# Kernel optimization log

Measured on AMD Instinct MI355X. Metric: run time of the kernel, lower is better.

## Reference

```python
import jax, jax.numpy as jnp
import numpy as np
from jax import lax

B, N, C = 16, 1024, 768
HID = 128           # route_hidden_dim (Cattn bottleneck + router hidden)
OUT = 2304          # qkv out_feature


def setup_inputs() -> dict:
    key = jax.random.key(0)
    ks = jax.random.split(key, 16)
    s = 0.02
    return {
        "input":  jax.random.normal(ks[0], (B, N, C), jnp.float32),
        "H": 32,
        "W": 32,
        "input2": jax.random.normal(ks[1], (B, N, C), jnp.float32),
        # qkv linear
        "qkv_w": jax.random.normal(ks[2], (OUT, C), jnp.float32) * s,
        "qkv_b": jax.random.normal(ks[3], (OUT,), jnp.float32) * s,
        # Cattn (vida_refine): fc1 -> dwconv -> gelu -> fc2
        "fc1_w": jax.random.normal(ks[4], (HID, C), jnp.float32) * s,
        "fc1_b": jnp.zeros((HID,), jnp.float32),
        "dw_w":  jax.random.normal(ks[5], (HID, 1, 3, 3), jnp.float32) * np.sqrt(2.0 / 9.0),
        "dw_b":  jnp.zeros((HID,), jnp.float32),
        "fc2_w": jax.random.normal(ks[6], (C, HID), jnp.float32) * s,
        "fc2_b": jnp.zeros((C,), jnp.float32),
        # router MLP: 1 -> HID -> 2
        "r1_w": jax.random.normal(ks[7], (HID, 1), jnp.float32) * s,
        "r1_b": jnp.zeros((HID,), jnp.float32),
        "r2_w": jax.random.normal(ks[8], (2, HID), jnp.float32) * s,
        "r2_b": jnp.zeros((2,), jnp.float32),
    }


def _linear(x, w, b):
    return jnp.einsum("bnc,oc->bno", x, w) + b


def _cattn(x, H, W, fc1_w, fc1_b, dw_w, dw_b, fc2_w, fc2_b):
    # fc1 -> depthwise 3x3 conv over HxW -> GELU(exact) -> fc2
    x = _linear(x, fc1_w, fc1_b)                       # [B,N,HID]
    b, n, h = x.shape
    xi = x.transpose(0, 2, 1).reshape(b, h, H, W)      # [B,HID,H,W]
    xi = lax.conv_general_dilated(
        xi, dw_w, window_strides=(1, 1), padding="SAME",
        feature_group_count=h,
        dimension_numbers=("NCHW", "OIHW", "NCHW"),
    ) + dw_b[None, :, None, None]
    x = xi.reshape(b, h, n).transpose(0, 2, 1)         # [B,N,HID]
    x = jax.nn.gelu(x, approximate=False)              # torch nn.GELU default = erf
    return _linear(x, fc2_w, fc2_b)                    # [B,N,C]


def _get_logit(inp, refine_x2):
    # cosine sim between per-batch token-mean of `inp` and refine_x2, then
    # per-batch min-max normalization (skipped when max == min)
    mean = jnp.mean(inp, axis=1, keepdims=True)        # [B,1,C]
    dot = jnp.sum(refine_x2 * mean, axis=-1, keepdims=True)
    n1 = jnp.linalg.norm(mean, axis=-1, keepdims=True)
    n2 = jnp.linalg.norm(refine_x2, axis=-1, keepdims=True)
    csim = dot / (n1 * n2)                             # [B,N,1]
    mn = jnp.min(csim, axis=1, keepdims=True)
    mx = jnp.max(csim, axis=1, keepdims=True)
    rng = mx - mn
    return jnp.where(rng != 0, (csim - mn) / jnp.where(rng != 0, rng, 1.0), csim)


def reference(input, H, W, input2, qkv_w, qkv_b, fc1_w, fc1_b, dw_w, dw_b,
              fc2_w, fc2_b, r1_w, r1_b, r2_w, r2_b):
    q1 = _linear(input, qkv_w, qkv_b)                              # [B,N,OUT]
    refine_x2 = input2 + _cattn(input2, H, W, fc1_w, fc1_b, dw_w, dw_b, fc2_w, fc2_b)
    q2 = _linear(refine_x2, qkv_w, qkv_b)                          # [B,N,OUT]
    csim = _get_logit(input, refine_x2)                            # [B,N,1]
    h = jax.nn.relu(_linear(csim, r1_w, r1_b))                     # [B,N,HID]
    logits = jax.nn.sigmoid(_linear(h, r2_w, r2_b))                # [B,N,2]
    # gumbel_softmax(hard=False, tau=1) with a fixed key for determinism
    g = jax.random.gumbel(jax.random.key(42), logits.shape, logits.dtype)
    router = jax.nn.softmax(logits + g, axis=-1)[:, :, 0]          # [B,N]
    return (q1, q2, router)
```

## Files before the change

kernel.cpp:

```cpp
#include <hip/hip_runtime.h>
#include <cstdint>
#include <cstddef>

#define BQ 16
#define NT 1024
#define CH 768
#define HIDN 128
#define OUTF 2304
#define MTOT (BQ*NT)

typedef __attribute__((ext_vector_type(4))) float f32x4;
typedef __attribute__((ext_vector_type(8))) short short8;

__device__ __forceinline__ unsigned short f2bf(float f){
  unsigned u = __float_as_uint(f);
  u += 0x7FFFu + ((u >> 16) & 1u);
  return (unsigned short)(u >> 16);
}
__device__ __forceinline__ float bf2f(unsigned short h){
  return __uint_as_float(((unsigned)h) << 16);
}

__device__ __forceinline__ void gload16(const void* g, void* l){
  __builtin_amdgcn_global_load_lds((const __attribute__((address_space(1))) void*)g,
                                   (__attribute__((address_space(3))) void*)l, 16, 0, 0);
}

__device__ __forceinline__ void mfma16(f32x4& d, short8 a, short8 b){
  asm volatile("v_mfma_f32_16x16x32_bf16 %0, %1, %2, %0" : "+v"(d) : "v"(a), "v"(b));
}

__global__ void k_f2bf_all(const float* __restrict__ in0, const float* __restrict__ in1,
                           const float* __restrict__ in2, const float* __restrict__ in3,
                           const float* __restrict__ in4,
                           unsigned short* __restrict__ o0, unsigned short* __restrict__ o1,
                           unsigned short* __restrict__ o2, unsigned short* __restrict__ o3,
                           unsigned short* __restrict__ o4)
{
  const long step = (long)2048 * 256 * 4;
  for (long i = (long)(blockIdx.x * 256 + threadIdx.x) * 4; i < 27131904L; i += step){
    const float* s; unsigned short* d; long off;
    if      (i < 12582912L){ s = in0; d = o0; off = i; }
    else if (i < 25165824L){ s = in1; d = o1; off = i - 12582912L; }
    else if (i < 26935296L){ s = in2; d = o2; off = i - 25165824L; }
    else if (i < 27033600L){ s = in3; d = o3; off = i - 26935296L; }
    else                   { s = in4; d = o4; off = i - 27033600L; }
    float4 v = *reinterpret_cast<const float4*>(s + off);
    ushort4 o;
    o.x = f2bf(v.x); o.y = f2bf(v.y); o.z = f2bf(v.z); o.w = f2bf(v.w);
    *reinterpret_cast<ushort4*>(d + off) = o;
  }
}

#define STAGE(matB_, buf_, h_, t_) { \
    const unsigned short* g_ = ((matB_) ? Bbase : Abase) + (size_t)(h_)*128*K + (size_t)(t_)*64; \
    char* d_ = ldsWaveDst + (matB_)*65536 + (buf_)*32768 + (h_)*16384; \
    gload16(g_, d_); \
    gload16(g_ + rowK64, d_ + 8192); \
  }

#define PH_OPEN() \
    asm volatile("s_barrier" ::: "memory"); \
    asm volatile("s_waitcnt lgkmcnt(0)" ::: "memory"); \
    __builtin_amdgcn_sched_barrier(0); \
    __builtin_amdgcn_s_setprio(1);

#define PH_CLOSE() \
    __builtin_amdgcn_s_setprio(0); \
    asm volatile("s_barrier" ::: "memory");

#define MF16(mb, nb, BV) \
    _Pragma("unroll") \
    for (int ks = 0; ks < 2; ++ks) \
      _Pragma("unroll") \
      for (int mf = 0; mf < 4; ++mf) \
        _Pragma("unroll") \
        for (int nf = 0; nf < 2; ++nf) \
          mfma16(acc[(mb)+mf][(nb)+nf], av[mf][ks], BV[nf][ks]);

#define TILE(t_, b_) { \
    const int t = (t_); const int b = (b_); \
    _Pragma("unroll") for (int mf = 0; mf < 4; ++mf){ av[mf][0]=ldA(b,mf,0); av[mf][1]=ldA(b,mf,1); } \
    _Pragma("unroll") for (int nf = 0; nf < 2; ++nf){ b0v[nf][0]=ldB(b,nf,0); b0v[nf][1]=ldB(b,nf,1); } \
    if (t+1 < T) STAGE(0, b^1, 1, t+1); \
    PH_OPEN(); MF16(0,0,b0v); PH_CLOSE(); \
    _Pragma("unroll") for (int nf = 0; nf < 2; ++nf){ b1v[nf][0]=ldB(b,2+nf,0); b1v[nf][1]=ldB(b,2+nf,1); } \
    if (t+1 < T) STAGE(1, b^1, 0, t+1); \
    PH_OPEN(); MF16(0,2,b1v); PH_CLOSE(); \
    _Pragma("unroll") for (int mf = 0; mf < 4; ++mf){ av[mf][0]=ldA(b,4+mf,0); av[mf][1]=ldA(b,4+mf,1); } \
    if (t+2 < T) STAGE(0, b, 0, t+2); \
    PH_OPEN(); MF16(4,2,b1v); PH_CLOSE(); \
    if (t+2 < T) STAGE(1, b, 1, t+2); \
    PH_OPEN(); MF16(4,0,b0v); \
    __builtin_amdgcn_s_setprio(0); \
    if (t+2 < T) { asm volatile("s_waitcnt vmcnt(4)" ::: "memory"); } \
    else         { asm volatile("s_waitcnt vmcnt(0)" ::: "memory"); } \
    asm volatile("s_barrier" ::: "memory"); \
  }

template<int T>
__device__ __forceinline__
void gemm256_body(char* lds8,
                  const unsigned short* __restrict__ A,
                  const unsigned short* __restrict__ B,
                  const float* __restrict__ bias,
                  float* __restrict__ C,
                  int N, int K, int nbn, int bid, int nwg)
{
  const int tid = threadIdx.x;
  const int ln = tid & 63, wv = tid >> 6;
  const int wm = wv >> 2, wn = wv & 3;
  const int llo = ln & 15, lhi = ln >> 4;

  const int cpx = nwg >> 3;
  const int swz = (bid & 7) * cpx + (bid >> 3);
  const int bm = swz / nbn, bn = swz % nbn;
  const int m0 = bm * 256, n0 = bn * 256;

  const int srow = tid >> 3;
  const int sslot = (tid & 7) ^ (srow & 7);
  const unsigned short* Abase = A + (size_t)(m0 + srow) * K + sslot * 8;
  const unsigned short* Bbase = B + (size_t)(n0 + srow) * K + sslot * 8;
  const size_t rowK64 = (size_t)64 * K;
  char* ldsWaveDst = lds8 + (wv << 10);

  const int swz0 = ((lhi ^ (ln & 7)) << 4);
  const char* aRd0 = lds8 + (wm*64 + llo)*128 + swz0;
  const char* aRd1 = lds8 + (wm*64 + llo)*128 + (swz0 ^ 64);
  const char* bRd0 = lds8 + 65536 + (wn*32 + llo)*128 + swz0;
  const char* bRd1 = lds8 + 65536 + (wn*32 + llo)*128 + (swz0 ^ 64);

  auto ldA = [&](int b, int mf, int ks) -> short8 {
    const char* p = (ks ? aRd1 : aRd0) + b*32768 + (mf>>2)*16384 + (mf&3)*2048;
    return *reinterpret_cast<const short8*>(p);
  };
  auto ldB = [&](int b, int nf, int ks) -> short8 {
    const char* p = (ks ? bRd1 : bRd0) + b*32768 + (nf>>1)*16384 + (nf&1)*2048;
    return *reinterpret_cast<const short8*>(p);
  };

  f32x4 acc[8][4];
  #pragma unroll
  for (int m = 0; m < 8; ++m)
    #pragma unroll
    for (int n = 0; n < 4; ++n) acc[m][n] = 0.0f;

  STAGE(0, 0, 0, 0);
  STAGE(1, 0, 1, 0);
  STAGE(0, 0, 1, 0);
  STAGE(1, 0, 0, 0);
  STAGE(0, 1, 0, 1);
  STAGE(1, 1, 1, 1);
  asm volatile("s_waitcnt vmcnt(4)" ::: "memory");
  asm volatile("s_barrier" ::: "memory");

  short8 av[4][2], b0v[2][2], b1v[2][2];
  #pragma unroll 1
  for (int t0 = 0; t0 < T; t0 += 2){
    TILE(t0,   0);
    TILE(t0+1, 1);
  }

  asm volatile("s_nop 7\n\ts_nop 7\n\ts_nop 7" ::: );

  #pragma unroll
  for (int mf = 0; mf < 8; ++mf){
    const int row = m0 + (mf>>2)*128 + wm*64 + (mf&3)*16 + lhi*4;
    #pragma unroll
    for (int j = 0; j < 4; ++j){
      #pragma unroll
      for (int nf = 0; nf < 4; ++nf){
        const int col = n0 + (nf>>1)*128 + wn*32 + (nf&1)*16 + llo;
        C[(size_t)(row + j) * N + col] = acc[mf][nf][j] + bias[col];
      }
    }
  }
}

__device__ __forceinline__
void fc1_body(char* lds, const unsigned short* __restrict__ A,
              const unsigned short* __restrict__ B,
              const float* __restrict__ bias, unsigned short* __restrict__ Cb, int fb)
{
  const int tid = threadIdx.x;
  if (tid >= 256){
    #pragma unroll 1
    for (int i = 0; i < 24; ++i){ __syncthreads(); __syncthreads(); }
    return;
  }
  unsigned short (*sA)[32] = (unsigned short(*)[32])lds;
  unsigned short (*sB)[32] = (unsigned short(*)[32])(lds + 8192);
  const int wv = tid >> 6, ln = tid & 63;
  const int wr = wv >> 1, wc = wv & 1;
  const int lhi = ln >> 4, llo = ln & 15;
  const int m0 = fb * 128;
  const int N = 128, K = 768;

  f32x4 acc[4][4];
  #pragma unroll
  for (int m = 0; m < 4; ++m)
    #pragma unroll
    for (int n = 0; n < 4; ++n) acc[m][n] = 0.0f;

  const int lrow = ln >> 2;
  const int lk8  = (ln & 3) * 8;

  #pragma unroll 1
  for (int kt = 0; kt < 768; kt += 32){
    #pragma unroll
    for (int cc = 0; cc < 2; ++cc){
      int c = wv * 2 + cc;
      gload16(A + (size_t)(m0 + c*16 + lrow) * K + kt + lk8, &sA[c*16][0]);
      gload16(B + (size_t)(c*16 + lrow) * K + kt + lk8, &sB[c*16][0]);
    }
    __syncthreads();

    short8 av[4], bv[4];
    #pragma unroll
    for (int m = 0; m < 4; ++m)
      av[m] = *reinterpret_cast<const short8*>(&sA[wr*64 + m*16 + llo][lhi*8]);
    #pragma unroll
    for (int n = 0; n < 4; ++n)
      bv[n] = *reinterpret_cast<const short8*>(&sB[wc*64 + n*16 + llo][lhi*8]);

    #pragma unroll
    for (int m = 0; m < 4; ++m)
      #pragma unroll
      for (int n = 0; n < 4; ++n)
        mfma16(acc[m][n], bv[n], av[m]);
    __syncthreads();
  }

  asm volatile("s_nop 7\n\ts_nop 7\n\ts_nop 7" ::: );

  float4 bias4[4];
  #pragma unroll
  for (int n = 0; n < 4; ++n)
    bias4[n] = *reinterpret_cast<const float4*>(&bias[wc*64 + n*16 + lhi*4]);

  #pragma unroll
  for (int m = 0; m < 4; ++m){
    const int row = m0 + wr*64 + m*16 + llo;
    #pragma unroll
    for (int n = 0; n < 4; ++n){
      const int colbase = wc*64 + n*16 + lhi*4;
      ushort4 o;
      o.x = f2bf(acc[m][n][0] + bias4[n].x);
      o.y = f2bf(acc[m][n][1] + bias4[n].y);
      o.z = f2bf(acc[m][n][2] + bias4[n].z);
      o.w = f2bf(acc[m][n][3] + bias4[n].w);
      *reinterpret_cast<ushort4*>(&Cb[(size_t)row * N + colbase]) = o;
    }
  }
}

__device__ __forceinline__
void mean_body(char* lds, const unsigned short* __restrict__ x1b,
               float* __restrict__ meanb, float* __restrict__ n1p, int mbid)
{
  float (*tmp)[128] = (float(*)[128])lds;
  const int b = mbid / 6, cg = mbid % 6;
  const int tid = threadIdx.x;
  const int oct = tid & 15, rg = tid >> 4;
  const unsigned short* ip = x1b + (size_t)b*NT*CH + (size_t)rg*32*CH + cg*128 + oct*8;

  float s[8];
  #pragma unroll
  for (int j = 0; j < 8; ++j) s[j] = 0.f;
  #pragma unroll 4
  for (int r = 0; r < 32; ++r){
    short8 v = *reinterpret_cast<const short8*>(ip + (size_t)r*CH);
    #pragma unroll
    for (int j = 0; j < 8; ++j) s[j] += bf2f((unsigned short)v[j]);
  }
  #pragma unroll
  for (int j = 0; j < 8; ++j) tmp[rg][oct*8 + j] = s[j];
  __syncthreads();

  if (tid < 128){
    float m = 0.f;
    #pragma unroll
    for (int g = 0; g < 32; ++g) m += tmp[g][tid];
    m *= (1.0f/1024.0f);
    meanb[b*CH + cg*128 + tid] = m;
    float q = m * m;
    for (int off = 32; off; off >>= 1) q += __shfl_down(q, off, 64);
    if ((tid & 63) == 0) n1p[b*12 + cg*2 + (tid >> 6)] = q;
  }
}

__device__ __forceinline__ void threefry(unsigned k0, unsigned k1, unsigned x0, unsigned x1,
                                         unsigned& o0, unsigned& o1){
  unsigned ks2 = k0 ^ k1 ^ 0x1BD11BDAu;
  x0 += k0; x1 += k1;
#define TFR(r) { x0 += x1; x1 = (x1 << r) | (x1 >> (32 - r)); x1 ^= x0; }
  TFR(13) TFR(15) TFR(26) TFR(6)  x0 += k1;  x1 += ks2 + 1u;
  TFR(17) TFR(29) TFR(16) TFR(24) x0 += ks2; x1 += k0 + 2u;
  TFR(13) TFR(15) TFR(26) TFR(6)  x0 += k0;  x1 += k1 + 3u;
  TFR(17) TFR(29) TFR(16) TFR(24) x0 += k1;  x1 += ks2 + 4u;
  TFR(13) TFR(15) TFR(26) TFR(6)  x0 += ks2; x1 += k0 + 5u;
#undef TFR
  o0 = x0; o1 = x1;
}

__device__ __forceinline__ float gumbel_from_bits(unsigned bits){
  float f = __uint_as_float((bits >> 9) | 0x3F800000u) - 1.0f;
  const float TINY = 1.17549435e-38f;
  float u = fmaxf(TINY, f + TINY);
  return -logf(-logf(u));
}

__device__ __forceinline__
void router_body(char* lds, const float* __restrict__ part, const float* __restrict__ n1p,
                 const float* __restrict__ r1w, const float* __restrict__ r1b,
                 const float* __restrict__ r2w, const float* __restrict__ r2b,
                 float* __restrict__ out, int b)
{
  float* cs   = (float*)lds;
  float* red  = (float*)(lds + 4096);
  float* w1s  = (float*)(lds + 4096 + 64);
  float* b1s  = w1s + HIDN;
  float* w20s = b1s + HIDN;
  float* w21s = w20s + HIDN;
  const int tid = threadIdx.x;
  if (tid < HIDN){
    w1s[tid]  = r1w[tid];
    b1s[tid]  = r1b[tid];
    w20s[tid] = r2w[tid];
    w21s[tid] = r2w[HIDN + tid];
  }
  float n1s = 0.f;
  #pragma unroll
  for (int s = 0; s < 12; ++s) n1s += n1p[b*12 + s];
  float n1 = sqrtf(n1s);
  float lmin = 3.4e38f, lmax = -3.4e38f;
  #pragma unroll
  for (int j = 0; j < 2; ++j){
    int tk = tid + j*512;
    int t = b*NT + tk;
    float dot = 0.f, q = 0.f;
    #pragma unroll
    for (int s = 0; s < 12; ++s){
      dot += part[(size_t)s * MTOT + t];
      q   += part[(size_t)(12 + s) * MTOT + t];
    }
    float v = dot / (n1 * sqrtf(q));
    cs[tk] = v;
    lmin = fminf(lmin, v); lmax = fmaxf(lmax, v);
  }
  int ln = tid & 63, wv = tid >> 6;
  for (int off = 32; off; off >>= 1){
    lmin = fminf(lmin, __shfl_down(lmin, off, 64));
    lmax = fmaxf(lmax, __shfl_down(lmax, off, 64));
  }
  if (ln == 0){ red[wv] = lmin; red[8+wv] = lmax; }
  __syncthreads();
  float mn = red[0], mx = red[8];
  #pragma unroll
  for (int s = 1; s < 8; ++s){ mn = fminf(mn, red[s]); mx = fmaxf(mx, red[8+s]); }
  float rng = mx - mn;
  bool nz = (rng != 0.0f);

  const float r2b0 = r2b[0], r2b1 = r2b[1];
  float v[2], l0[2], l1[2];
  #pragma unroll
  for (int j = 0; j < 2; ++j){
    float c0 = cs[tid + j*512];
    v[j] = nz ? (c0 - mn) / rng : c0;
    l0[j] = r2b0; l1[j] = r2b1;
  }
  for (int k = 0; k < HIDN; ++k){
    float a = w1s[k], bb = b1s[k], c0 = w20s[k], c1 = w21s[k];
    #pragma unroll
    for (int j = 0; j < 2; ++j){
      float hh = fmaxf(v[j] * a + bb, 0.f);
      l0[j] += hh * c0;
      l1[j] += hh * c1;
    }
  }
  #pragma unroll
  for (int j = 0; j < 2; ++j){
    float s0 = 1.f / (1.f + expf(-l0[j]));
    float s1 = 1.f / (1.f + expf(-l1[j]));
    int t = b*NT + tid + j*512;
    unsigned o0, o1;
    threefry(0u, 42u, 0u, (unsigned)(2*t),     o0, o1);
    float g0 = gumbel_from_bits(o0 ^ o1);
    threefry(0u, 42u, 0u, (unsigned)(2*t + 1), o0, o1);
    float g1 = gumbel_from_bits(o0 ^ o1);
    out[t] = 1.f / (1.f + expf((s1 + g1) - (s0 + g0)));
  }
}

__global__ __launch_bounds__(512, 2)
void k_combo1(const unsigned short* __restrict__ xrb, const unsigned short* __restrict__ w1b,
              const float* __restrict__ fc1_b, unsigned short* __restrict__ t1dst,
              const unsigned short* __restrict__ x1b,
              float* __restrict__ meanb, float* __restrict__ n1p)
{
  __shared__ __align__(1024) char lds8[131072];
  const int bid = blockIdx.x;
  if (bid < 128){
    fc1_body(lds8, xrb, w1b, fc1_b, t1dst, bid);
  } else {
    mean_body(lds8, x1b, meanb, n1p, bid - 128);
  }
}

__global__ __launch_bounds__(512, 2)
void k_combo2(const unsigned short* __restrict__ Aall, const unsigned short* __restrict__ wqb,
              const float* __restrict__ qkv_b, float* __restrict__ q1q2,
              const float* __restrict__ part, const float* __restrict__ n1p,
              const float* __restrict__ r1w, const float* __restrict__ r1b,
              const float* __restrict__ r2w, const float* __restrict__ r2b,
              float* __restrict__ router)
{
  __shared__ __align__(1024) char lds8[131072];
  const int bid = blockIdx.x;
  if (bid < 1152){
    gemm256_body<CH/64>(lds8, Aall, wqb, qkv_b, q1q2, OUTF, CH, OUTF/256, bid, 1152);
  } else {
    router_body(lds8, part, n1p, r1w, r1b, r2w, r2b, router, bid - 1152);
  }
}

__global__ __launch_bounds__(256, 2)
void k_gemm_fc2(const unsigned short* __restrict__ A, const unsigned short* __restrict__ B,
                const float* __restrict__ bias, const unsigned short* __restrict__ addb,
                unsigned short* __restrict__ Cb,
                const float* __restrict__ meanb, float* __restrict__ part,
                int M, int N, int K)
{
  __shared__ unsigned short sA[128][32];
  __shared__ unsigned short sB[128][32];
  const int tid = threadIdx.x;
  const int wv = tid >> 6, ln = tid & 63;
  const int wr = wv >> 1, wc = wv & 1;
  const int lhi = ln >> 4, llo = ln & 15;
  const int m0 = blockIdx.x * 128, n0 = blockIdx.y * 128;

  f32x4 acc[4][4];
  #pragma unroll
  for (int m = 0; m < 4; ++m)
    #pragma unroll
    for (int n = 0; n < 4; ++n) acc[m][n] = 0.0f;

  const int lrow = ln >> 2;
  const int lk8  = (ln & 3) * 8;

  for (int kt = 0; kt < K; kt += 32){
    #pragma unroll
    for (int cc = 0; cc < 2; ++cc){
      int c = wv * 2 + cc;
      gload16(A + (size_t)(m0 + c*16 + lrow) * K + kt + lk8, &sA[c*16][0]);
      gload16(B + (size_t)(n0 + c*16 + lrow) * K + kt + lk8, &sB[c*16][0]);
    }
    __syncthreads();

    short8 av[4], bv[4];
    #pragma unroll
    for (int m = 0; m < 4; ++m)
      av[m] = *reinterpret_cast<const short8*>(&sA[wr*64 + m*16 + llo][lhi*8]);
    #pragma unroll
    for (int n = 0; n < 4; ++n)
      bv[n] = *reinterpret_cast<const short8*>(&sB[wc*64 + n*16 + llo][lhi*8]);

    #pragma unroll
    for (int m = 0; m < 4; ++m)
      #pragma unroll
      for (int n = 0; n < 4; ++n)
        mfma16(acc[m][n], bv[n], av[m]);
    __syncthreads();
  }

  asm volatile("s_nop 7\n\ts_nop 7\n\ts_nop 7" ::: );

  float4 bias4[4];
  #pragma unroll
  for (int n = 0; n < 4; ++n)
    bias4[n] = *reinterpret_cast<const float4*>(&bias[n0 + wc*64 + n*16 + lhi*4]);

  const int bb = m0 >> 10;
  const float* mp = meanb + bb * CH;
  float4 mp4[4];
  #pragma unroll
  for (int n = 0; n < 4; ++n)
    mp4[n] = *reinterpret_cast<const float4*>(&mp[n0 + wc*64 + n*16 + lhi*4]);

  #pragma unroll
  for (int m = 0; m < 4; ++m){
    const int row = m0 + wr*64 + m*16 + llo;
    float dsum = 0.f, qsum = 0.f;
    #pragma unroll
    for (int n = 0; n < 4; ++n){
      const int colbase = n0 + wc*64 + n*16 + lhi*4;
      ushort4 a4 = *reinterpret_cast<const ushort4*>(&addb[(size_t)row * N + colbase]);
      float v0 = acc[m][n][0] + bias4[n].x + bf2f(a4.x);
      float v1 = acc[m][n][1] + bias4[n].y + bf2f(a4.y);
      float v2 = acc[m][n][2] + bias4[n].z + bf2f(a4.z);
      float v3 = acc[m][n][3] + bias4[n].w + bf2f(a4.w);
      ushort4 o; o.x = f2bf(v0); o.y = f2bf(v1); o.z = f2bf(v2); o.w = f2bf(v3);
      *reinterpret_cast<ushort4*>(&Cb[(size_t)row * N + colbase]) = o;
      dsum += v0*mp4[n].x + v1*mp4[n].y + v2*mp4[n].z + v3*mp4[n].w;
      qsum += v0*v0 + v1*v1 + v2*v2 + v3*v3;
    }
    dsum += __shfl_xor(dsum, 16, 64);  qsum += __shfl_xor(qsum, 16, 64);
    dsum += __shfl_xor(dsum, 32, 64);  qsum += __shfl_xor(qsum, 32, 64);
    if (ln < 16){
      const int slot = blockIdx.y * 2 + wc;
      part[(size_t)slot * MTOT + row] = dsum;
      part[(size_t)(12 + slot) * MTOT + row] = qsum;
    }
  }
}

__global__ void k_dwgelu(const unsigned short* __restrict__ t1b, const float* __restrict__ dww,
                         const float* __restrict__ dwb, unsigned short* __restrict__ t2)
{
  int idx = blockIdx.x * blockDim.x + threadIdx.x;
  int hq = idx & 31; int t = idx >> 5;
  int h = hq * 4;
  int n = t & (NT-1); int b = t >> 10;
  int y = n >> 5, x = n & 31;

  float w[4][9];
  #pragma unroll
  for (int i = 0; i < 4; ++i)
    #pragma unroll
    for (int k = 0; k < 9; ++k) w[i][k] = dww[(h+i)*9 + k];

  float a0 = dwb[h+0], a1 = dwb[h+1], a2 = dwb[h+2], a3 = dwb[h+3];
  #pragma unroll
  for (int dy = -1; dy <= 1; ++dy){
    int yy = y + dy; if ((unsigned)yy >= 32u) continue;
    #pragma unroll
    for (int dx = -1; dx <= 1; ++dx){
      int xx = x + dx; if ((unsigned)xx >= 32u) continue;
      ushort4 v = *reinterpret_cast<const ushort4*>(&t1b[((size_t)b*NT + yy*32 + xx)*HIDN + h]);
      int k = (dy+1)*3 + (dx+1);
      a0 += bf2f(v.x) * w[0][k]; a1 += bf2f(v.y) * w[1][k];
      a2 += bf2f(v.z) * w[2][k]; a3 += bf2f(v.w) * w[3][k];
    }
  }
  const float is2 = 0.70710678118654752440f;
  a0 = 0.5f*a0*(1.0f + erff(a0*is2));
  a1 = 0.5f*a1*(1.0f + erff(a1*is2));
  a2 = 0.5f*a2*(1.0f + erff(a2*is2));
  a3 = 0.5f*a3*(1.0f + erff(a3*is2));
  ushort4 o; o.x = f2bf(a0); o.y = f2bf(a1); o.z = f2bf(a2); o.w = f2bf(a3);
  *reinterpret_cast<ushort4*>(&t2[(size_t)t*HIDN + h]) = o;
}

extern "C" void kernel_launch(void* const* d_in, const int* in_sizes, int n_in,
                              void* d_out, int out_size, void* d_ws, size_t ws_size,
                              hipStream_t stream)
{
  (void)in_sizes; (void)n_in; (void)out_size;
  const float* input  = (const float*)d_in[0];
  const float* input2 = (const float*)d_in[3];
  const float* qkv_w  = (const float*)d_in[4];
  const float* qkv_b  = (const float*)d_in[5];
  const float* fc1_w  = (const float*)d_in[6];
  const float* fc1_b  = (const float*)d_in[7];
  const float* dw_w   = (const float*)d_in[8];
  const float* dw_b   = (const float*)d_in[9];
  const float* fc2_w  = (const float*)d_in[10];
  const float* fc2_b  = (const float*)d_in[11];
  const float* r1_w   = (const float*)d_in[12];
  const float* r1_b   = (const float*)d_in[13];
  const float* r2_w   = (const float*)d_in[14];
  const float* r2_b   = (const float*)d_in[15];

  float* q1 = (float*)d_out;
  float* router = q1 + (size_t)2 * MTOT * OUTF;

  if (ws_size < 67000000u) return;

  char* ws = (char*)d_ws;
  unsigned short* x1b = (unsigned short*)ws; ws += (size_t)MTOT*CH*2;
  unsigned short* xrb = (unsigned short*)ws; ws += (size_t)MTOT*CH*2;
  unsigned short* wqb = (unsigned short*)ws; ws += (size_t)OUTF*CH*2;
  unsigned short* w1b = (unsigned short*)ws; ws += (size_t)HIDN*CH*2;
  unsigned short* w2b = (unsigned short*)ws; ws += (size_t)CH*HIDN*2;
  unsigned short* t1b = (unsigned short*)ws; ws += (size_t)MTOT*HIDN*4;
  unsigned short* t2  = (unsigned short*)ws; ws += (size_t)MTOT*HIDN*2;
  float*          mb  = (float*)ws;          ws += (size_t)BQ*CH*4;
  float*          n1p = (float*)ws;          ws += 1024;
  float*          part= (float*)t1b;

  k_f2bf_all<<<dim3(2048), 256, 0, stream>>>(
      input, input2, qkv_w, fc1_w, fc2_w, x1b, xrb, wqb, w1b, w2b);

  unsigned short* t1dst = t1b + (size_t)MTOT*HIDN;
  k_combo1<<<dim3(224), 512, 0, stream>>>(
      xrb, w1b, fc1_b, t1dst, x1b, mb, n1p);

  k_dwgelu<<<dim3(MTOT*32/256), 256, 0, stream>>>(t1dst, dw_w, dw_b, t2);

  k_gemm_fc2<<<dim3(MTOT/128, CH/128), 256, 0, stream>>>(
      t2, w2b, fc2_b, xrb, xrb, mb, part, MTOT, CH, HIDN);

  k_combo2<<<dim3(1168), 512, 0, stream>>>(
      x1b, wqb, qkv_b, q1, part, n1p, r1_w, r1_b, r2_w, r2_b, router);
}
```

Measured before the change: 227.2 us.

## Fuse bf16 conversion, fc1 and mean into one kernel reading fp32 directly

Merges the fp32-to-bf16 conversion kernel with the fc1 GEMM and token-mean kernel into a single launch. fc1 and the mean now read the fp32 inputs directly, converting in registers before staging to LDS. The conversion of fc1_w is dropped and the remaining conversion blocks run alongside them. This removes one launch and the serial dependency between the conversion and fc1/mean, at the cost of fc1 reading twice as many bytes and losing the async global-to-LDS loads.

```diff
diff --git a/kernel.cpp b/kernel.cpp
--- a/kernel.cpp
+++ b/kernel.cpp
@@ -30,26 +30,11 @@
   asm volatile("v_mfma_f32_16x16x32_bf16 %0, %1, %2, %0" : "+v"(d) : "v"(a), "v"(b));
 }
 
-__global__ void k_f2bf_all(const float* __restrict__ in0, const float* __restrict__ in1,
-                           const float* __restrict__ in2, const float* __restrict__ in3,
-                           const float* __restrict__ in4,
-                           unsigned short* __restrict__ o0, unsigned short* __restrict__ o1,
-                           unsigned short* __restrict__ o2, unsigned short* __restrict__ o3,
-                           unsigned short* __restrict__ o4)
-{
-  const long step = (long)2048 * 256 * 4;
-  for (long i = (long)(blockIdx.x * 256 + threadIdx.x) * 4; i < 27131904L; i += step){
-    const float* s; unsigned short* d; long off;
-    if      (i < 12582912L){ s = in0; d = o0; off = i; }
-    else if (i < 25165824L){ s = in1; d = o1; off = i - 12582912L; }
-    else if (i < 26935296L){ s = in2; d = o2; off = i - 25165824L; }
-    else if (i < 27033600L){ s = in3; d = o3; off = i - 26935296L; }
-    else                   { s = in4; d = o4; off = i - 27033600L; }
-    float4 v = *reinterpret_cast<const float4*>(s + off);
-    ushort4 o;
-    o.x = f2bf(v.x); o.y = f2bf(v.y); o.z = f2bf(v.z); o.w = f2bf(v.w);
-    *reinterpret_cast<ushort4*>(d + off) = o;
-  }
+__device__ __forceinline__ short8 pack8(float4 a, float4 b){
+  short8 p;
+  p[0]=(short)f2bf(a.x); p[1]=(short)f2bf(a.y); p[2]=(short)f2bf(a.z); p[3]=(short)f2bf(a.w);
+  p[4]=(short)f2bf(b.x); p[5]=(short)f2bf(b.y); p[6]=(short)f2bf(b.z); p[7]=(short)f2bf(b.w);
+  return p;
 }
 
 #define STAGE(matB_, buf_, h_, t_) { \
@@ -178,41 +163,39 @@
 }
 
 __device__ __forceinline__
-void fc1_body(char* lds, const unsigned short* __restrict__ A,
-              const unsigned short* __restrict__ B,
-              const float* __restrict__ bias, unsigned short* __restrict__ Cb, int fb)
-{
-  const int tid = threadIdx.x;
-  if (tid >= 256){
-    #pragma unroll 1
-    for (int i = 0; i < 24; ++i){ __syncthreads(); __syncthreads(); }
-    return;
-  }
+void fc1f32_body(char* lds, const float* __restrict__ A, const float* __restrict__ B,
+                 const float* __restrict__ bias, unsigned short* __restrict__ Cb, int fb)
+{
   unsigned short (*sA)[32] = (unsigned short(*)[32])lds;
   unsigned short (*sB)[32] = (unsigned short(*)[32])(lds + 8192);
+  const int tid = threadIdx.x;
   const int wv = tid >> 6, ln = tid & 63;
   const int wr = wv >> 1, wc = wv & 1;
   const int lhi = ln >> 4, llo = ln & 15;
   const int m0 = fb * 128;
-  const int N = 128, K = 768;
+  const int N = 128;
+  const int srow = tid >> 1, scol = (tid & 1) * 16;
+  const float* Ap = A + (size_t)(m0 + srow) * 768 + scol;
+  const float* Bp = B + (size_t)srow * 768 + scol;
 
   f32x4 acc[4][4];
   #pragma unroll
   for (int m = 0; m < 4; ++m)
     #pragma unroll
     for (int n = 0; n < 4; ++n) acc[m][n] = 0.0f;
-
-  const int lrow = ln >> 2;
-  const int lk8  = (ln & 3) * 8;
 
   #pragma unroll 1
   for (int kt = 0; kt < 768; kt += 32){
-    #pragma unroll
-    for (int cc = 0; cc < 2; ++cc){
-      int c = wv * 2 + cc;
-      gload16(A + (size_t)(m0 + c*16 + lrow) * K + kt + lk8, &sA[c*16][0]);
-      gload16(B + (size_t)(c*16 + lrow) * K + kt + lk8, &sB[c*16][0]);
-    }
+    float4 a4[4], b4[4];
+    #pragma unroll
+    for (int j = 0; j < 4; ++j){
+      a4[j] = *reinterpret_cast<const float4*>(Ap + kt + j*4);
+      b4[j] = *reinterpret_cast<const float4*>(Bp + kt + j*4);
+    }
+    *reinterpret_cast<short8*>(&sA[srow][scol])     = pack8(a4[0], a4[1]);
+    *reinterpret_cast<short8*>(&sA[srow][scol + 8]) = pack8(a4[2], a4[3]);
+    *reinterpret_cast<short8*>(&sB[srow][scol])     = pack8(b4[0], b4[1]);
+    *reinterpret_cast<short8*>(&sB[srow][scol + 8]) = pack8(b4[2], b4[3]);
     __syncthreads();
 
     short8 av[4], bv[4];
@@ -255,23 +238,24 @@
 }
 
 __device__ __forceinline__
-void mean_body(char* lds, const unsigned short* __restrict__ x1b,
-               float* __restrict__ meanb, float* __restrict__ n1p, int mbid)
+void meanf32_body(char* lds, const float* __restrict__ input,
+                  float* __restrict__ meanb, float* __restrict__ n1p, int mbid)
 {
   float (*tmp)[128] = (float(*)[128])lds;
   const int b = mbid / 6, cg = mbid % 6;
   const int tid = threadIdx.x;
   const int oct = tid & 15, rg = tid >> 4;
-  const unsigned short* ip = x1b + (size_t)b*NT*CH + (size_t)rg*32*CH + cg*128 + oct*8;
+  const float* ip = input + (size_t)b*NT*CH + (size_t)rg*64*CH + cg*128 + oct*8;
 
   float s[8];
   #pragma unroll
   for (int j = 0; j < 8; ++j) s[j] = 0.f;
-  #pragma unroll 4
-  for (int r = 0; r < 32; ++r){
-    short8 v = *reinterpret_cast<const short8*>(ip + (size_t)r*CH);
-    #pragma unroll
-    for (int j = 0; j < 8; ++j) s[j] += bf2f((unsigned short)v[j]);
+  #pragma unroll 2
+  for (int r = 0; r < 64; ++r){
+    float4 v0 = *reinterpret_cast<const float4*>(ip + (size_t)r*CH);
+    float4 v1 = *reinterpret_cast<const float4*>(ip + (size_t)r*CH + 4);
+    s[0]+=v0.x; s[1]+=v0.y; s[2]+=v0.z; s[3]+=v0.w;
+    s[4]+=v1.x; s[5]+=v1.y; s[6]+=v1.z; s[7]+=v1.w;
   }
   #pragma unroll
   for (int j = 0; j < 8; ++j) tmp[rg][oct*8 + j] = s[j];
@@ -280,12 +264,42 @@
   if (tid < 128){
     float m = 0.f;
     #pragma unroll
-    for (int g = 0; g < 32; ++g) m += tmp[g][tid];
+    for (int g = 0; g < 16; ++g) m += tmp[g][tid];
     m *= (1.0f/1024.0f);
     meanb[b*CH + cg*128 + tid] = m;
     float q = m * m;
     for (int off = 32; off; off >>= 1) q += __shfl_down(q, off, 64);
     if ((tid & 63) == 0) n1p[b*12 + cg*2 + (tid >> 6)] = q;
+  }
+}
+
+__global__ void k_mega(const float* __restrict__ input, const float* __restrict__ input2,
+                       const float* __restrict__ qkv_w, const float* __restrict__ fc2_w,
+                       unsigned short* __restrict__ x1b, unsigned short* __restrict__ xrb,
+                       unsigned short* __restrict__ wqb, unsigned short* __restrict__ w2b,
+                       const float* __restrict__ fc1_w, const float* __restrict__ fc1_b,
+                       unsigned short* __restrict__ t1dst,
+                       float* __restrict__ meanb, float* __restrict__ n1p)
+{
+  __shared__ __align__(64) char lds[16384];
+  const int bid = blockIdx.x;
+  if (bid < 128){
+    fc1f32_body(lds, input2, fc1_w, fc1_b, t1dst, bid);
+  } else if (bid < 224){
+    meanf32_body(lds, input, meanb, n1p, bid - 128);
+  } else {
+    const long step = (long)2048 * 256 * 4;
+    for (long i = (long)((bid - 224) * 256 + threadIdx.x) * 4; i < 27033600L; i += step){
+      const float* s; unsigned short* d; long off;
+      if      (i < 12582912L){ s = input;  d = x1b; off = i; }
+      else if (i < 25165824L){ s = input2; d = xrb; off = i - 12582912L; }
+      else if (i < 26935296L){ s = qkv_w;  d = wqb; off = i - 25165824L; }
+      else                   { s = fc2_w;  d = w2b; off = i - 26935296L; }
+      float4 v = *reinterpret_cast<const float4*>(s + off);
+      ushort4 o;
+      o.x = f2bf(v.x); o.y = f2bf(v.y); o.z = f2bf(v.z); o.w = f2bf(v.w);
+      *reinterpret_cast<ushort4*>(d + off) = o;
+    }
   }
 }
 
@@ -389,21 +403,6 @@
     threefry(0u, 42u, 0u, (unsigned)(2*t + 1), o0, o1);
     float g1 = gumbel_from_bits(o0 ^ o1);
     out[t] = 1.f / (1.f + expf((s1 + g1) - (s0 + g0)));
-  }
-}
-
-__global__ __launch_bounds__(512, 2)
-void k_combo1(const unsigned short* __restrict__ xrb, const unsigned short* __restrict__ w1b,
-              const float* __restrict__ fc1_b, unsigned short* __restrict__ t1dst,
-              const unsigned short* __restrict__ x1b,
-              float* __restrict__ meanb, float* __restrict__ n1p)
-{
-  __shared__ __align__(1024) char lds8[131072];
-  const int bid = blockIdx.x;
-  if (bid < 128){
-    fc1_body(lds8, xrb, w1b, fc1_b, t1dst, bid);
-  } else {
-    mean_body(lds8, x1b, meanb, n1p, bid - 128);
   }
 }
 
@@ -580,7 +579,7 @@
   unsigned short* x1b = (unsigned short*)ws; ws += (size_t)MTOT*CH*2;
   unsigned short* xrb = (unsigned short*)ws; ws += (size_t)MTOT*CH*2;
   unsigned short* wqb = (unsigned short*)ws; ws += (size_t)OUTF*CH*2;
-  unsigned short* w1b = (unsigned short*)ws; ws += (size_t)HIDN*CH*2;
+  ws += (size_t)HIDN*CH*2;
   unsigned short* w2b = (unsigned short*)ws; ws += (size_t)CH*HIDN*2;
   unsigned short* t1b = (unsigned short*)ws; ws += (size_t)MTOT*HIDN*4;
   unsigned short* t2  = (unsigned short*)ws; ws += (size_t)MTOT*HIDN*2;
@@ -588,12 +587,10 @@
   float*          n1p = (float*)ws;          ws += 1024;
   float*          part= (float*)t1b;
 
-  k_f2bf_all<<<dim3(2048), 256, 0, stream>>>(
-      input, input2, qkv_w, fc1_w, fc2_w, x1b, xrb, wqb, w1b, w2b);
-
   unsigned short* t1dst = t1b + (size_t)MTOT*HIDN;
-  k_combo1<<<dim3(224), 512, 0, stream>>>(
-      xrb, w1b, fc1_b, t1dst, x1b, mb, n1p);
+  k_mega<<<dim3(2272), 256, 0, stream>>>(
+      input, input2, qkv_w, fc2_w, x1b, xrb, wqb, w2b,
+      fc1_w, fc1_b, t1dst, mb, n1p);
 
   k_dwgelu<<<dim3(MTOT*32/256), 256, 0, stream>>>(t1dst, dw_w, dw_b, t2);
 
```

After: 233.7 us, median of 2. +2.9%, slower.
